# Performance work log

Hardware: AMD Instinct MI355X
Metric: run time of the kernel (lower is better)

Reference implementation:

```python
import jax, jax.numpy as jnp
import numpy as np

CI = 1024
CO = 1024
B, S = 16, 2048

def setup_inputs() -> dict:
    key = jax.random.key(0)
    k1, k2, k3, k4 = jax.random.split(key, 4)
    x = jax.random.normal(k1, (B, S, CI), dtype=jnp.float16)
    # true int8 weights stored as int8
    weight_int8 = jax.random.randint(k2, (CO, CI), -128, 128, dtype=jnp.int32).astype(jnp.int8)
    weight_scale = jax.random.uniform(k3, (CO,), dtype=jnp.float32, minval=1e-3, maxval=1e-2)
    act_scale = jnp.float32(0.02)
    bias = jax.random.normal(k4, (CO,), dtype=jnp.float32) * 0.1
    return {"x": x, "weight_int8": weight_int8, "weight_scale": weight_scale,
            "act_scale": act_scale, "bias": bias}

def reference(x, weight_int8, weight_scale, act_scale, bias):
    orig_shape = x.shape
    orig_dtype = x.dtype
    x2d = x.reshape(-1, orig_shape[-1])  # (M, Ci)
    # 1) dynamic activation quantization to int8
    x_int8 = jnp.clip(jnp.round(x2d.astype(jnp.float32) / act_scale), -128, 127).astype(jnp.int8)
    # 2) true int8 GEMM with int32 accumulation (torch._int_mm)
    y_int32 = jnp.matmul(x_int8, weight_int8.T, preferred_element_type=jnp.int32)  # (M, Co)
    # 3) dequant with fused output scale (act_scale * per-row weight_scale) + bias
    output_scale = (act_scale * weight_scale).astype(jnp.float32)  # (Co,)
    y = y_int32.astype(jnp.float32) * output_scale[None, :] + bias.astype(jnp.float32)[None, :]
    return y.reshape(*orig_shape[:-1], weight_int8.shape[0]).astype(orig_dtype)
```

## Files before the change

### kernel.cpp

```cpp
#include <hip/hip_runtime.h>
#include <stdint.h>

#define K_DIM 1024
#define N_DIM 1024
#define BM 128
#define BN 128
#define BK 64
#define NKT (K_DIM / BK)
#define TILE_BYTES (BM * BK)
#define W_BLOCKS 256
#define XQ_BLOCKS 2048
#define LDA 80

typedef int v4i __attribute__((ext_vector_type(4)));

__device__ __forceinline__ int quant1(float f, float inv) {
    return (int)fminf(fmaxf(rintf(f * inv), -128.f), 127.f);
}
__device__ __forceinline__ uint32_t pack4(int a, int b, int c, int d) {
    return (uint32_t)(a & 255) | ((uint32_t)(b & 255) << 8) |
           ((uint32_t)(c & 255) << 16) | ((uint32_t)(d & 255) << 24);
}
__device__ __forceinline__ int swz(int r, int c) {
    return (r * BK + c) ^ ((r & 7) << 4);
}
__device__ __forceinline__ bool probe_x_is_f32(const void* xptr) {
    const uint16_t* xu = (const uint16_t*)xptr;
    int lane = (int)(threadIdx.x & 63);
    float pv = __uint_as_float(((uint32_t)xu[2 * lane]) << 16);
    float pa = fabsf(pv);
    unsigned long long mx = __ballot(pa >= 0.125f && pa < 2.0f);
    return (__popcll(mx) < 32);
}

__global__ __launch_bounds__(256) void prep_kernel(
    const void* __restrict__ xptr,
    const int*  __restrict__ w32,
    const float* __restrict__ ascale_p,
    uint8_t* __restrict__ xq,
    uint8_t* __restrict__ wq,
    int M)
{
    const float inv = 1.0f / ascale_p[0];
    const int tid = threadIdx.x;

    if (blockIdx.x < W_BLOCKS) {
        int c = blockIdx.x * 256 + tid;
        int q = c & 3;
        int r = (c >> 2) & 127;
        int t = c >> 9;
        size_t row = (size_t)(t >> 4) * BM + r;
        int    col = (t & 15) * BK + q * 16;
        const int4* src = (const int4*)(w32 + row * K_DIM + col);
        uint32_t pk[4];
#pragma unroll
        for (int g = 0; g < 4; g++) {
            int4 v = src[g];
            pk[g] = pack4(v.x, v.y, v.z, v.w);
        }
        *(uint4*)(wq + ((size_t)t << 13) + swz(r, q * 16)) =
            make_uint4(pk[0], pk[1], pk[2], pk[3]);
        return;
    }

    const bool x_is_f32 = probe_x_is_f32(xptr);
    const int c0 = (blockIdx.x - W_BLOCKS) * 256 + tid;
    const int stride = XQ_BLOCKS * 256;

    if (x_is_f32) {
        float4 v[4][4];
        int rr[4], qq[4], tt[4];
#pragma unroll
        for (int it = 0; it < 4; it++) {
            int c = c0 + it * stride;
            qq[it] = c & 3;
            rr[it] = (c >> 2) & 127;
            tt[it] = c >> 9;
            const float4* src = (const float4*)((const float*)xptr +
                ((size_t)(tt[it] >> 4) * BM + rr[it]) * K_DIM +
                (tt[it] & 15) * BK + qq[it] * 16);
#pragma unroll
            for (int g = 0; g < 4; g++) v[it][g] = src[g];
        }
#pragma unroll
        for (int it = 0; it < 4; it++) {
            uint32_t pk[4];
#pragma unroll
            for (int g = 0; g < 4; g++) {
                float4 w = v[it][g];
                pk[g] = pack4(quant1(w.x, inv), quant1(w.y, inv),
                              quant1(w.z, inv), quant1(w.w, inv));
            }
            *(uint4*)(xq + ((size_t)tt[it] << 13) + swz(rr[it], qq[it] * 16)) =
                make_uint4(pk[0], pk[1], pk[2], pk[3]);
        }
    } else {
        const int XC = M * (K_DIM / 16);
        for (int c = c0; c < XC; c += stride) {
            int q = c & 3;
            int r = (c >> 2) & 127;
            int t = c >> 9;
            size_t row = (size_t)(t >> 4) * BM + r;
            int    col = (t & 15) * BK + q * 16;
            const uint4* src = (const uint4*)((const uint16_t*)xptr + row * K_DIM + col);
            union { uint4 v[2]; uint32_t u[8]; } ax;
            ax.v[0] = src[0]; ax.v[1] = src[1];
            uint32_t pk[4];
#pragma unroll
            for (int i = 0; i < 4; i++) {
                uint32_t wa = ax.u[2 * i], wb = ax.u[2 * i + 1];
                pk[i] = pack4(quant1(__uint_as_float(wa << 16), inv),
                              quant1(__uint_as_float(wa & 0xffff0000u), inv),
                              quant1(__uint_as_float(wb << 16), inv),
                              quant1(__uint_as_float(wb & 0xffff0000u), inv));
            }
            *(uint4*)(xq + ((size_t)t << 13) + swz(r, q * 16)) =
                make_uint4(pk[0], pk[1], pk[2], pk[3]);
        }
    }
}

__global__ __launch_bounds__(256, 2) void int8_gemm_kernel(
    const uint8_t* __restrict__ xq,
    const uint8_t* __restrict__ wq,
    const float* __restrict__ wscale,
    const float* __restrict__ ascale_p,
    const float* __restrict__ bias,
    float* __restrict__ out)
{
    const int tid  = threadIdx.x;
    const int lane = tid & 63;
    const int wave = tid >> 6;
    const int wm   = wave >> 1;
    const int wn   = wave & 1;
    const int quad = lane >> 4;
    const int l16  = lane & 15;

    const int numm = (int)gridDim.x >> 3;
    const int logical = ((int)blockIdx.x & 7) * numm + ((int)blockIdx.x >> 3);
    const int mblk = logical >> 3;
    const int nblk = logical & 7;

    const uint8_t* pA = xq + (size_t)mblk * (NKT * TILE_BYTES);
    const uint8_t* pB = wq + (size_t)nblk * (NKT * TILE_BYTES);

    int offA[4], offB[4];
#pragma unroll
    for (int i = 0; i < 4; i++) {
        offA[i] = swz(wm * 64 + i * 16 + l16, quad * 16);
        offB[i] = swz(wn * 64 + i * 16 + l16, quad * 16);
    }

    v4i acc[4][4] = {};

#pragma unroll
    for (int kb = 0; kb < NKT; kb++) {
        const uint8_t* tA = pA + (size_t)kb * TILE_BYTES;
        const uint8_t* tB = pB + (size_t)kb * TILE_BYTES;
        v4i af[4], bf[4];
#pragma unroll
        for (int i = 0; i < 4; i++) {
            af[i] = *(const v4i*)(tA + offA[i]);
            bf[i] = *(const v4i*)(tB + offB[i]);
        }
#pragma unroll
        for (int mt = 0; mt < 4; mt++)
#pragma unroll
            for (int nt = 0; nt < 4; nt++)
                acc[mt][nt] = __builtin_amdgcn_mfma_i32_16x16x64_i8(
                    af[mt], bf[nt], acc[mt][nt], 0, 0, 0);
    }

    const float s = ascale_p[0];
    const int m0 = mblk * BM, n0 = nblk * BN;
    float osc[4], obi[4];
#pragma unroll
    for (int nt = 0; nt < 4; nt++) {
        int col = n0 + wn * 64 + nt * 16 + l16;
        osc[nt] = s * wscale[col];
        obi[nt] = bias[col];
    }
#pragma unroll
    for (int mt = 0; mt < 4; mt++) {
        int rowb = m0 + wm * 64 + mt * 16 + quad * 4;
#pragma unroll
        for (int nt = 0; nt < 4; nt++) {
            int col = n0 + wn * 64 + nt * 16 + l16;
#pragma unroll
            for (int r = 0; r < 4; r++) {
                out[(size_t)(rowb + r) * N_DIM + col] =
                    (float)acc[mt][nt][r] * osc[nt] + obi[nt];
            }
        }
    }
}

template<bool X_F32>
__device__ __forceinline__ void gemm_body(
    int8_t* lA, int8_t* lB,
    const void* __restrict__ xptr,
    const int* __restrict__ w32,
    const float* __restrict__ wscale,
    const float s,
    const float* __restrict__ bias,
    float* __restrict__ out)
{
    const int tid  = threadIdx.x;
    const int lane = tid & 63;
    const int wave = tid >> 6;
    const int wm   = wave >> 1;
    const int wn   = wave & 1;
    const int quad = lane >> 4;
    const int l16  = lane & 15;

    const int mblk = (int)blockIdx.x >> 3;
    const int nblk = (int)blockIdx.x & 7;
    const int m0 = mblk * BM;
    const int n0 = nblk * BN;

    const float inv = 1.0f / s;
    const int ar = tid >> 1;
    const int ah = (tid & 1) * 32;

    const float*    xrowf = (const float*)xptr    + (size_t)(m0 + ar) * K_DIM + ah;
    const uint16_t* xrowh = (const uint16_t*)xptr + (size_t)(m0 + ar) * K_DIM + ah;
    const int*      wrow  = w32 + (size_t)(n0 + ar) * K_DIM + ah;

    v4i acc[4][4] = {};

    for (int kb = 0; kb < K_DIM; kb += BK) {
        {
            uint32_t pk[8];
            if (X_F32) {
                const float4* xs = (const float4*)(xrowf + kb);
#pragma unroll
                for (int g = 0; g < 8; g++) {
                    float4 v = xs[g];
                    pk[g] = pack4(quant1(v.x, inv), quant1(v.y, inv),
                                  quant1(v.z, inv), quant1(v.w, inv));
                }
            } else {
                const uint4* xs = (const uint4*)(xrowh + kb);
                union { uint4 v[4]; uint32_t u[16]; } ax;
                ax.v[0] = xs[0]; ax.v[1] = xs[1]; ax.v[2] = xs[2]; ax.v[3] = xs[3];
#pragma unroll
                for (int i = 0; i < 8; i++) {
                    uint32_t wa = ax.u[2 * i], wb = ax.u[2 * i + 1];
                    pk[i] = pack4(quant1(__uint_as_float(wa << 16), inv),
                                  quant1(__uint_as_float(wa & 0xffff0000u), inv),
                                  quant1(__uint_as_float(wb << 16), inv),
                                  quant1(__uint_as_float(wb & 0xffff0000u), inv));
                }
            }
            uint4* adst = (uint4*)&lA[ar * LDA + ah];
            adst[0] = make_uint4(pk[0], pk[1], pk[2], pk[3]);
            adst[1] = make_uint4(pk[4], pk[5], pk[6], pk[7]);
        }
        {
            const int4* ws4 = (const int4*)(wrow + kb);
            uint32_t pb[8];
#pragma unroll
            for (int g = 0; g < 8; g++) {
                int4 v = ws4[g];
                pb[g] = pack4(v.x, v.y, v.z, v.w);
            }
            uint4* bdst = (uint4*)&lB[ar * LDA + ah];
            bdst[0] = make_uint4(pb[0], pb[1], pb[2], pb[3]);
            bdst[1] = make_uint4(pb[4], pb[5], pb[6], pb[7]);
        }
        __syncthreads();

        v4i af[4], bf[4];
#pragma unroll
        for (int mt = 0; mt < 4; mt++)
            af[mt] = *(const v4i*)&lA[(wm * 64 + mt * 16 + l16) * LDA + quad * 16];
#pragma unroll
        for (int nt = 0; nt < 4; nt++)
            bf[nt] = *(const v4i*)&lB[(wn * 64 + nt * 16 + l16) * LDA + quad * 16];
#pragma unroll
        for (int mt = 0; mt < 4; mt++)
#pragma unroll
            for (int nt = 0; nt < 4; nt++)
                acc[mt][nt] = __builtin_amdgcn_mfma_i32_16x16x64_i8(af[mt], bf[nt], acc[mt][nt], 0, 0, 0);
        __syncthreads();
    }

    float osc[4], obi[4];
#pragma unroll
    for (int nt = 0; nt < 4; nt++) {
        int col = n0 + wn * 64 + nt * 16 + l16;
        osc[nt] = s * wscale[col];
        obi[nt] = bias[col];
    }
#pragma unroll
    for (int mt = 0; mt < 4; mt++) {
        int rowb = m0 + wm * 64 + mt * 16 + quad * 4;
#pragma unroll
        for (int nt = 0; nt < 4; nt++) {
            int col = n0 + wn * 64 + nt * 16 + l16;
#pragma unroll
            for (int r = 0; r < 4; r++) {
                out[(size_t)(rowb + r) * N_DIM + col] =
                    (float)acc[mt][nt][r] * osc[nt] + obi[nt];
            }
        }
    }
}

__global__ __launch_bounds__(256, 2) void int8_linear_fused(
    const void* __restrict__ xptr,
    const int* __restrict__ w32,
    const float* __restrict__ wscale,
    const float* __restrict__ ascale_p,
    const float* __restrict__ bias,
    float* __restrict__ out)
{
    __shared__ int8_t lA[BM * LDA];
    __shared__ int8_t lB[BN * LDA];
    const bool x_is_f32 = probe_x_is_f32(xptr);
    const float s = ascale_p[0];
    if (x_is_f32) gemm_body<true >(lA, lB, xptr, w32, wscale, s, bias, out);
    else          gemm_body<false>(lA, lB, xptr, w32, wscale, s, bias, out);
}

extern "C" void kernel_launch(void* const* d_in, const int* in_sizes, int n_in,
                              void* d_out, int out_size, void* d_ws, size_t ws_size,
                              hipStream_t stream) {
    const void*  xptr   = d_in[0];
    const int*   w32    = (const int*)d_in[1];
    const float* wscale = (const float*)d_in[2];
    const float* ascale = (const float*)d_in[3];
    const float* bias   = (const float*)d_in[4];
    float*       out    = (float*)d_out;

    int M = in_sizes[0] / K_DIM;
    size_t need = (size_t)M * K_DIM + (size_t)N_DIM * K_DIM;

    bool split_ok = (d_ws != nullptr) && (ws_size >= need) &&
                    (M == 32768) && (M % BM == 0);

    if (split_ok) {
        uint8_t* xq = (uint8_t*)d_ws;
        uint8_t* wq = xq + (size_t)M * K_DIM;
        prep_kernel<<<dim3(W_BLOCKS + XQ_BLOCKS), 256, 0, stream>>>(
            xptr, w32, ascale, xq, wq, M);
        int numm = M / BM;
        int8_gemm_kernel<<<dim3(numm * 8), 256, 0, stream>>>(
            xq, wq, wscale, ascale, bias, out);
    } else {
        dim3 grid((M / BM) * (N_DIM / BN));
        int8_linear_fused<<<grid, 256, 0, stream>>>(
            xptr, w32, wscale, ascale, bias, out);
    }
}
```

Baseline: 284.1 us.

## Fuse activation quantization into GEMM with full-K row-strip LDS residency

Replaces the separate activation-quantize prep pass and the tiled GEMM with a single kernel. Each block quantizes a 64-row strip of activations into shared memory, covering the full K and overlapped with the first N-tile's MFMA loop, then sweeps all eight N-tiles reading pre-packed int8 weights directly from global memory. This removes the round trip of writing and re-reading the quantized activation buffer. In exchange it uses 64 KB of LDS per block, which lowers occupancy, and it reloads the weight fragments from global or L2 without LDS staging.

```diff
diff --git a/kernel.cpp b/kernel.cpp
--- a/kernel.cpp
+++ b/kernel.cpp
@@ -3,13 +3,8 @@
 
 #define K_DIM 1024
 #define N_DIM 1024
-#define BM 128
-#define BN 128
-#define BK 64
-#define NKT (K_DIM / BK)
-#define TILE_BYTES (BM * BK)
-#define W_BLOCKS 256
-#define XQ_BLOCKS 2048
+#define NKT 16
+#define WTILE 8192
 #define LDA 80
 
 typedef int v4i __attribute__((ext_vector_type(4)));
@@ -22,7 +17,7 @@
            ((uint32_t)(c & 255) << 16) | ((uint32_t)(d & 255) << 24);
 }
 __device__ __forceinline__ int swz(int r, int c) {
-    return (r * BK + c) ^ ((r & 7) << 4);
+    return (r * 64 + c) ^ ((r & 7) << 4);
 }
 __device__ __forceinline__ bool probe_x_is_f32(const void* xptr) {
     const uint16_t* xu = (const uint16_t*)xptr;
@@ -33,98 +28,33 @@
     return (__popcll(mx) < 32);
 }
 
-__global__ __launch_bounds__(256) void prep_kernel(
+__global__ __launch_bounds__(256) void prep_w_kernel(
+    const int* __restrict__ w32, uint8_t* __restrict__ wq)
+{
+    int c = blockIdx.x * 256 + threadIdx.x;
+    int q = c & 3;
+    int r = (c >> 2) & 127;
+    int t = c >> 9;
+    size_t row = (size_t)(t >> 4) * 128 + r;
+    int    col = (t & 15) * 64 + q * 16;
+    const int4* src = (const int4*)(w32 + row * K_DIM + col);
+    uint32_t pk[4];
+#pragma unroll
+    for (int g = 0; g < 4; g++) {
+        int4 v = src[g];
+        pk[g] = pack4(v.x, v.y, v.z, v.w);
+    }
+    *(uint4*)(wq + ((size_t)t << 13) + swz(r, q * 16)) =
+        make_uint4(pk[0], pk[1], pk[2], pk[3]);
+}
+
+template<bool X_F32>
+__device__ __forceinline__ void fused_body(
+    uint8_t (*lA)[4096],
     const void* __restrict__ xptr,
-    const int*  __restrict__ w32,
-    const float* __restrict__ ascale_p,
-    uint8_t* __restrict__ xq,
-    uint8_t* __restrict__ wq,
-    int M)
-{
-    const float inv = 1.0f / ascale_p[0];
-    const int tid = threadIdx.x;
-
-    if (blockIdx.x < W_BLOCKS) {
-        int c = blockIdx.x * 256 + tid;
-        int q = c & 3;
-        int r = (c >> 2) & 127;
-        int t = c >> 9;
-        size_t row = (size_t)(t >> 4) * BM + r;
-        int    col = (t & 15) * BK + q * 16;
-        const int4* src = (const int4*)(w32 + row * K_DIM + col);
-        uint32_t pk[4];
-#pragma unroll
-        for (int g = 0; g < 4; g++) {
-            int4 v = src[g];
-            pk[g] = pack4(v.x, v.y, v.z, v.w);
-        }
-        *(uint4*)(wq + ((size_t)t << 13) + swz(r, q * 16)) =
-            make_uint4(pk[0], pk[1], pk[2], pk[3]);
-        return;
-    }
-
-    const bool x_is_f32 = probe_x_is_f32(xptr);
-    const int c0 = (blockIdx.x - W_BLOCKS) * 256 + tid;
-    const int stride = XQ_BLOCKS * 256;
-
-    if (x_is_f32) {
-        float4 v[4][4];
-        int rr[4], qq[4], tt[4];
-#pragma unroll
-        for (int it = 0; it < 4; it++) {
-            int c = c0 + it * stride;
-            qq[it] = c & 3;
-            rr[it] = (c >> 2) & 127;
-            tt[it] = c >> 9;
-            const float4* src = (const float4*)((const float*)xptr +
-                ((size_t)(tt[it] >> 4) * BM + rr[it]) * K_DIM +
-                (tt[it] & 15) * BK + qq[it] * 16);
-#pragma unroll
-            for (int g = 0; g < 4; g++) v[it][g] = src[g];
-        }
-#pragma unroll
-        for (int it = 0; it < 4; it++) {
-            uint32_t pk[4];
-#pragma unroll
-            for (int g = 0; g < 4; g++) {
-                float4 w = v[it][g];
-                pk[g] = pack4(quant1(w.x, inv), quant1(w.y, inv),
-                              quant1(w.z, inv), quant1(w.w, inv));
-            }
-            *(uint4*)(xq + ((size_t)tt[it] << 13) + swz(rr[it], qq[it] * 16)) =
-                make_uint4(pk[0], pk[1], pk[2], pk[3]);
-        }
-    } else {
-        const int XC = M * (K_DIM / 16);
-        for (int c = c0; c < XC; c += stride) {
-            int q = c & 3;
-            int r = (c >> 2) & 127;
-            int t = c >> 9;
-            size_t row = (size_t)(t >> 4) * BM + r;
-            int    col = (t & 15) * BK + q * 16;
-            const uint4* src = (const uint4*)((const uint16_t*)xptr + row * K_DIM + col);
-            union { uint4 v[2]; uint32_t u[8]; } ax;
-            ax.v[0] = src[0]; ax.v[1] = src[1];
-            uint32_t pk[4];
-#pragma unroll
-            for (int i = 0; i < 4; i++) {
-                uint32_t wa = ax.u[2 * i], wb = ax.u[2 * i + 1];
-                pk[i] = pack4(quant1(__uint_as_float(wa << 16), inv),
-                              quant1(__uint_as_float(wa & 0xffff0000u), inv),
-                              quant1(__uint_as_float(wb << 16), inv),
-                              quant1(__uint_as_float(wb & 0xffff0000u), inv));
-            }
-            *(uint4*)(xq + ((size_t)t << 13) + swz(r, q * 16)) =
-                make_uint4(pk[0], pk[1], pk[2], pk[3]);
-        }
-    }
-}
-
-__global__ __launch_bounds__(256, 2) void int8_gemm_kernel(
-    const uint8_t* __restrict__ xq,
     const uint8_t* __restrict__ wq,
     const float* __restrict__ wscale,
-    const float* __restrict__ ascale_p,
+    const float s,
     const float* __restrict__ bias,
     float* __restrict__ out)
 {
@@ -136,63 +66,184 @@
     const int quad = lane >> 4;
     const int l16  = lane & 15;
 
-    const int numm = (int)gridDim.x >> 3;
-    const int logical = ((int)blockIdx.x & 7) * numm + ((int)blockIdx.x >> 3);
-    const int mblk = logical >> 3;
-    const int nblk = logical & 7;
-
-    const uint8_t* pA = xq + (size_t)mblk * (NKT * TILE_BYTES);
-    const uint8_t* pB = wq + (size_t)nblk * (NKT * TILE_BYTES);
-
-    int offA[4], offB[4];
-#pragma unroll
-    for (int i = 0; i < 4; i++) {
-        offA[i] = swz(wm * 64 + i * 16 + l16, quad * 16);
-        offB[i] = swz(wn * 64 + i * 16 + l16, quad * 16);
-    }
-
-    v4i acc[4][4] = {};
-
-#pragma unroll
-    for (int kb = 0; kb < NKT; kb++) {
-        const uint8_t* tA = pA + (size_t)kb * TILE_BYTES;
-        const uint8_t* tB = pB + (size_t)kb * TILE_BYTES;
-        v4i af[4], bf[4];
-#pragma unroll
-        for (int i = 0; i < 4; i++) {
-            af[i] = *(const v4i*)(tA + offA[i]);
-            bf[i] = *(const v4i*)(tB + offB[i]);
-        }
-#pragma unroll
-        for (int mt = 0; mt < 4; mt++)
+    const int mblk = (int)blockIdx.x;
+    const int m0   = mblk * 64;
+    const float inv = 1.0f / s;
+
+    const int qr = tid >> 2;
+    const int qc = (tid & 3) * 16;
+    const int wdst = swz(qr, qc);
+
+    const float*    xbf = (const float*)xptr    + (size_t)(m0 + qr) * K_DIM + qc;
+    const uint16_t* xbh = (const uint16_t*)xptr + (size_t)(m0 + qr) * K_DIM + qc;
+
+    int offA[2], offB[4];
+#pragma unroll
+    for (int mt = 0; mt < 2; mt++) offA[mt] = swz(wm * 32 + mt * 16 + l16, quad * 16);
+#pragma unroll
+    for (int nt = 0; nt < 4; nt++) offB[nt] = swz(wn * 64 + nt * 16 + l16, quad * 16);
+
+#pragma unroll
+    for (int kt = 0; kt < 4; kt++) {
+        uint32_t pk[4];
+        if (X_F32) {
+            const float4* s4 = (const float4*)(xbf + kt * 64);
+            float4 a = s4[0], b = s4[1], c = s4[2], d = s4[3];
+            pk[0] = pack4(quant1(a.x,inv),quant1(a.y,inv),quant1(a.z,inv),quant1(a.w,inv));
+            pk[1] = pack4(quant1(b.x,inv),quant1(b.y,inv),quant1(b.z,inv),quant1(b.w,inv));
+            pk[2] = pack4(quant1(c.x,inv),quant1(c.y,inv),quant1(c.z,inv),quant1(c.w,inv));
+            pk[3] = pack4(quant1(d.x,inv),quant1(d.y,inv),quant1(d.z,inv),quant1(d.w,inv));
+        } else {
+            const uint4* s4 = (const uint4*)(xbh + kt * 64);
+            union { uint4 v[2]; uint32_t u[8]; } ax;
+            ax.v[0] = s4[0]; ax.v[1] = s4[1];
+#pragma unroll
+            for (int i = 0; i < 4; i++) {
+                uint32_t wa = ax.u[2*i], wb = ax.u[2*i+1];
+                pk[i] = pack4(quant1(__uint_as_float(wa << 16), inv),
+                              quant1(__uint_as_float(wa & 0xffff0000u), inv),
+                              quant1(__uint_as_float(wb << 16), inv),
+                              quant1(__uint_as_float(wb & 0xffff0000u), inv));
+            }
+        }
+        *(uint4*)&lA[kt][wdst] = make_uint4(pk[0], pk[1], pk[2], pk[3]);
+    }
+    __syncthreads();
+
+    {
+        v4i acc[2][4] = {};
+#pragma unroll
+        for (int kb = 0; kb < NKT; kb++) {
+            float4 rf0, rf1, rf2, rf3; uint4 rh0, rh1;
+            if (kb < NKT - 4) {
+                if (X_F32) {
+                    const float4* s4 = (const float4*)(xbf + (kb + 4) * 64);
+                    rf0 = s4[0]; rf1 = s4[1]; rf2 = s4[2]; rf3 = s4[3];
+                } else {
+                    const uint4* s4 = (const uint4*)(xbh + (kb + 4) * 64);
+                    rh0 = s4[0]; rh1 = s4[1];
+                }
+            }
+            v4i af[2], bf[4];
+            af[0] = *(const v4i*)&lA[kb][offA[0]];
+            af[1] = *(const v4i*)&lA[kb][offA[1]];
+            const uint8_t* wt = wq + (size_t)kb * WTILE;
 #pragma unroll
             for (int nt = 0; nt < 4; nt++)
-                acc[mt][nt] = __builtin_amdgcn_mfma_i32_16x16x64_i8(
-                    af[mt], bf[nt], acc[mt][nt], 0, 0, 0);
-    }
-
-    const float s = ascale_p[0];
-    const int m0 = mblk * BM, n0 = nblk * BN;
-    float osc[4], obi[4];
-#pragma unroll
-    for (int nt = 0; nt < 4; nt++) {
-        int col = n0 + wn * 64 + nt * 16 + l16;
-        osc[nt] = s * wscale[col];
-        obi[nt] = bias[col];
-    }
-#pragma unroll
-    for (int mt = 0; mt < 4; mt++) {
-        int rowb = m0 + wm * 64 + mt * 16 + quad * 4;
+                bf[nt] = *(const v4i*)(wt + offB[nt]);
+#pragma unroll
+            for (int mt = 0; mt < 2; mt++)
+#pragma unroll
+                for (int nt = 0; nt < 4; nt++)
+                    acc[mt][nt] = __builtin_amdgcn_mfma_i32_16x16x64_i8(
+                        af[mt], bf[nt], acc[mt][nt], 0, 0, 0);
+            if (kb < NKT - 4) {
+                uint32_t pk[4];
+                if (X_F32) {
+                    pk[0] = pack4(quant1(rf0.x,inv),quant1(rf0.y,inv),quant1(rf0.z,inv),quant1(rf0.w,inv));
+                    pk[1] = pack4(quant1(rf1.x,inv),quant1(rf1.y,inv),quant1(rf1.z,inv),quant1(rf1.w,inv));
+                    pk[2] = pack4(quant1(rf2.x,inv),quant1(rf2.y,inv),quant1(rf2.z,inv),quant1(rf2.w,inv));
+                    pk[3] = pack4(quant1(rf3.x,inv),quant1(rf3.y,inv),quant1(rf3.z,inv),quant1(rf3.w,inv));
+                } else {
+                    uint32_t u[4] = { rh0.x, rh0.y, rh0.z, rh0.w };
+                    uint32_t v[4] = { rh1.x, rh1.y, rh1.z, rh1.w };
+#pragma unroll
+                    for (int i = 0; i < 2; i++) {
+                        uint32_t wa = u[2*i], wb = u[2*i+1];
+                        pk[i] = pack4(quant1(__uint_as_float(wa << 16), inv),
+                                      quant1(__uint_as_float(wa & 0xffff0000u), inv),
+                                      quant1(__uint_as_float(wb << 16), inv),
+                                      quant1(__uint_as_float(wb & 0xffff0000u), inv));
+                    }
+#pragma unroll
+                    for (int i = 0; i < 2; i++) {
+                        uint32_t wa = v[2*i], wb = v[2*i+1];
+                        pk[2+i] = pack4(quant1(__uint_as_float(wa << 16), inv),
+                                        quant1(__uint_as_float(wa & 0xffff0000u), inv),
+                                        quant1(__uint_as_float(wb << 16), inv),
+                                        quant1(__uint_as_float(wb & 0xffff0000u), inv));
+                    }
+                }
+                *(uint4*)&lA[kb + 4][wdst] = make_uint4(pk[0], pk[1], pk[2], pk[3]);
+            }
+            __syncthreads();
+        }
+        float osc[4], obi[4];
+#pragma unroll
+        for (int nt = 0; nt < 4; nt++) {
+            int col = wn * 64 + nt * 16 + l16;
+            osc[nt] = s * wscale[col];
+            obi[nt] = bias[col];
+        }
+#pragma unroll
+        for (int mt = 0; mt < 2; mt++) {
+            int rowb = m0 + wm * 32 + mt * 16 + quad * 4;
+#pragma unroll
+            for (int nt = 0; nt < 4; nt++) {
+                int col = wn * 64 + nt * 16 + l16;
+#pragma unroll
+                for (int r = 0; r < 4; r++)
+                    out[(size_t)(rowb + r) * N_DIM + col] =
+                        (float)acc[mt][nt][r] * osc[nt] + obi[nt];
+            }
+        }
+    }
+
+    for (int np = 1; np < 8; np++) {
+        const uint8_t* wbase = wq + (size_t)np * (NKT * WTILE);
+        v4i acc[2][4] = {};
+#pragma unroll
+        for (int kb = 0; kb < NKT; kb++) {
+            v4i af[2], bf[4];
+            af[0] = *(const v4i*)&lA[kb][offA[0]];
+            af[1] = *(const v4i*)&lA[kb][offA[1]];
+            const uint8_t* wt = wbase + (size_t)kb * WTILE;
+#pragma unroll
+            for (int nt = 0; nt < 4; nt++)
+                bf[nt] = *(const v4i*)(wt + offB[nt]);
+#pragma unroll
+            for (int mt = 0; mt < 2; mt++)
+#pragma unroll
+                for (int nt = 0; nt < 4; nt++)
+                    acc[mt][nt] = __builtin_amdgcn_mfma_i32_16x16x64_i8(
+                        af[mt], bf[nt], acc[mt][nt], 0, 0, 0);
+        }
+        const int n0 = np * 128;
+        float osc[4], obi[4];
 #pragma unroll
         for (int nt = 0; nt < 4; nt++) {
             int col = n0 + wn * 64 + nt * 16 + l16;
-#pragma unroll
-            for (int r = 0; r < 4; r++) {
-                out[(size_t)(rowb + r) * N_DIM + col] =
-                    (float)acc[mt][nt][r] * osc[nt] + obi[nt];
-            }
-        }
-    }
+            osc[nt] = s * wscale[col];
+            obi[nt] = bias[col];
+        }
+#pragma unroll
+        for (int mt = 0; mt < 2; mt++) {
+            int rowb = m0 + wm * 32 + mt * 16 + quad * 4;
+#pragma unroll
+            for (int nt = 0; nt < 4; nt++) {
+                int col = n0 + wn * 64 + nt * 16 + l16;
+#pragma unroll
+                for (int r = 0; r < 4; r++)
+                    out[(size_t)(rowb + r) * N_DIM + col] =
+                        (float)acc[mt][nt][r] * osc[nt] + obi[nt];
+            }
+        }
+    }
+}
+
+__global__ __launch_bounds__(256, 2) void fused_gemm_kernel(
+    const void* __restrict__ xptr,
+    const uint8_t* __restrict__ wq,
+    const float* __restrict__ wscale,
+    const float* __restrict__ ascale_p,
+    const float* __restrict__ bias,
+    float* __restrict__ out)
+{
+    __shared__ uint8_t lA[NKT][4096];
+    const bool x_is_f32 = probe_x_is_f32(xptr);
+    const float s = ascale_p[0];
+    if (x_is_f32) fused_body<true >(lA, xptr, wq, wscale, s, bias, out);
+    else          fused_body<false>(lA, xptr, wq, wscale, s, bias, out);
 }
 
 template<bool X_F32>
@@ -215,8 +266,8 @@
 
     const int mblk = (int)blockIdx.x >> 3;
     const int nblk = (int)blockIdx.x & 7;
-    const int m0 = mblk * BM;
-    const int n0 = nblk * BN;
+    const int m0 = mblk * 128;
+    const int n0 = nblk * 128;
 
     const float inv = 1.0f / s;
     const int ar = tid >> 1;
@@ -228,7 +279,7 @@
 
     v4i acc[4][4] = {};
 
-    for (int kb = 0; kb < K_DIM; kb += BK) {
+    for (int kb = 0; kb < K_DIM; kb += 64) {
         {
             uint32_t pk[8];
             if (X_F32) {
@@ -315,8 +366,8 @@
     const float* __restrict__ bias,
     float* __restrict__ out)
 {
-    __shared__ int8_t lA[BM * LDA];
-    __shared__ int8_t lB[BN * LDA];
+    __shared__ int8_t lA[128 * LDA];
+    __shared__ int8_t lB[128 * LDA];
     const bool x_is_f32 = probe_x_is_f32(xptr);
     const float s = ascale_p[0];
     if (x_is_f32) gemm_body<true >(lA, lB, xptr, w32, wscale, s, bias, out);
@@ -334,21 +385,17 @@
     float*       out    = (float*)d_out;
 
     int M = in_sizes[0] / K_DIM;
-    size_t need = (size_t)M * K_DIM + (size_t)N_DIM * K_DIM;
-
-    bool split_ok = (d_ws != nullptr) && (ws_size >= need) &&
-                    (M == 32768) && (M % BM == 0);
+    size_t need = (size_t)N_DIM * K_DIM;
+
+    bool split_ok = (d_ws != nullptr) && (ws_size >= need) && (M == 32768);
 
     if (split_ok) {
-        uint8_t* xq = (uint8_t*)d_ws;
-        uint8_t* wq = xq + (size_t)M * K_DIM;
-        prep_kernel<<<dim3(W_BLOCKS + XQ_BLOCKS), 256, 0, stream>>>(
-            xptr, w32, ascale, xq, wq, M);
-        int numm = M / BM;
-        int8_gemm_kernel<<<dim3(numm * 8), 256, 0, stream>>>(
-            xq, wq, wscale, ascale, bias, out);
+        uint8_t* wq = (uint8_t*)d_ws;
+        prep_w_kernel<<<dim3(256), 256, 0, stream>>>(w32, wq);
+        fused_gemm_kernel<<<dim3(M / 64), 256, 0, stream>>>(
+            xptr, wq, wscale, ascale, bias, out);
     } else {
-        dim3 grid((M / BM) * (N_DIM / BN));
+        dim3 grid((M / 128) * (N_DIM / 128));
         int8_linear_fused<<<grid, 256, 0, stream>>>(
             xptr, w32, wscale, ascale, bias, out);
     }
```

Result: slower. 309.4 us (+8.9%).
